# Performance work log

Hardware: AMD Instinct MI355X
Metric: run time of the kernel (lower is better)

The kernel has to match this reference:

```python
import jax, jax.numpy as jnp
import numpy as np

N_NODES = 500_000
N_EDGES = 8_000_000
NUM_GRAPHS = 512


def _glorot(key, shape):
    lim = float(np.sqrt(6.0 / (shape[0] + shape[1])))
    return jax.random.uniform(key, shape, jnp.float32, -lim, lim)


def setup_inputs() -> dict:
    key = jax.random.key(0)
    ks = jax.random.split(key, 10)
    x = jax.random.normal(ks[0], (N_NODES, 3), jnp.float32)
    edge_index = jax.random.randint(ks[1], (2, N_EDGES), 0, N_NODES, jnp.int64)
    batch = jnp.sort(jax.random.randint(ks[2], (N_NODES,), 0, NUM_GRAPHS, jnp.int64))
    return {
        "x": x,
        "edge_index": edge_index,
        "batch": batch,
        # GCNConv weights stored [in, out]; bias [out]
        "W1": _glorot(ks[3], (3, 16)),
        "b1": jnp.zeros((16,), jnp.float32),
        "W2": _glorot(ks[4], (16, 32)),
        "b2": jnp.zeros((32,), jnp.float32),
        "fW1": _glorot(ks[5], (32, 64)),
        "fb1": jnp.zeros((64,), jnp.float32),
        "fW2": _glorot(ks[6], (64, 3)),
        "fb2": jnp.zeros((3,), jnp.float32),
    }


def _gcn_conv(x, edge_index, W, b):
    n = x.shape[0]
    src, dst = edge_index[0], edge_index[1]
    h = x @ W  # [N, out]
    ones = jnp.ones((edge_index.shape[1],), h.dtype)
    deg = jax.ops.segment_sum(ones, dst, num_segments=n) + 1.0  # in-degree + self loop
    dinv = jax.lax.rsqrt(deg)
    norm = dinv[src] * dinv[dst]  # [E]
    agg = jax.ops.segment_sum(norm[:, None] * h[src], dst, num_segments=n)
    # self-loop contribution: norm_ii = dinv_i^2
    return agg + (dinv * dinv)[:, None] * h + b


def reference(x, edge_index, batch, W1, b1, W2, b2, fW1, fb1, fW2, fb2):
    h = jax.nn.relu(_gcn_conv(x, edge_index, W1, b1))
    h = jax.nn.relu(_gcn_conv(h, edge_index, W2, b2))
    # global_mean_pool over graph ids
    sums = jax.ops.segment_sum(h, batch, num_segments=NUM_GRAPHS)
    cnts = jax.ops.segment_sum(jnp.ones((h.shape[0],), h.dtype), batch, num_segments=NUM_GRAPHS)
    pooled = sums / jnp.maximum(cnts, 1.0)[:, None]  # [G, 32]
    z = jax.nn.relu(pooled @ fW1 + fb1)
    z = z @ fW2 + fb2
    return jax.nn.log_softmax(z, axis=1)
```

## Files before the change

kernel.cpp:

```cpp
#include <hip/hip_runtime.h>
#include <hip/hip_bf16.h>

constexpr int N_NODES    = 500000;
constexpr int N_EDGES    = 8000000;
constexpr int NUM_GRAPHS = 512;

constexpr int BSHIFT = 11;
constexpr int BSIZE  = 1 << BSHIFT;
constexpr int NBKT   = (N_NODES + BSIZE - 1) / BSIZE;
constexpr int EPB    = 8192;
constexpr int NBLK_A = (N_EDGES + EPB - 1) / EPB;
constexpr int NH     = NBKT * NBLK_A;
constexpr int SCAN_B = 256;
constexpr int NSB    = (NH + SCAN_B - 1) / SCAN_B;
constexpr int TSH    = 16;
constexpr int CAP    = 20480;

__device__ __forceinline__ float bf_lo(unsigned u) { return __uint_as_float(u << 16); }
__device__ __forceinline__ float bf_hi(unsigned u) { return __uint_as_float(u & 0xFFFF0000u); }
__device__ __forceinline__ unsigned short f2bf(float f) {
  unsigned u = __float_as_uint(f);
  return (unsigned short)((u + 0x7FFFu + ((u >> 16) & 1u)) >> 16);
}
__device__ __forceinline__ unsigned packbf(float a, float b) {
  return (unsigned)f2bf(a) | ((unsigned)f2bf(b) << 16);
}

__device__ __forceinline__ unsigned f2e4m3(float x) {
  x = fminf(x, 448.0f);
  unsigned xb = __float_as_uint(x);
  int e = (int)(xb >> 23) - 127;
  if (e < -6) {
    int m = (int)rintf(x * 512.0f);
    return (m <= 7) ? (unsigned)m : 0x08u;
  }
  unsigned lsb = (xb >> 20) & 1;
  unsigned r = xb + 0x7FFFFu + lsb;
  int e2 = (int)(r >> 23) - 127;
  unsigned m3 = (r >> 20) & 7;
  return (unsigned)(((e2 + 7) << 3) | m3);
}
__device__ __forceinline__ float e4m3f(unsigned b) {
  unsigned e = (b >> 3) & 0xF, m = b & 7;
  float norm = __uint_as_float(((e + 120u) << 23) | (m << 20));
  float den = (float)m * 0.001953125f;
  return e ? norm : den;
}

__global__ void k_hist(const int* __restrict__ dst, int* __restrict__ H) {
  __shared__ int h[NBKT];
  for (int i = threadIdx.x; i < NBKT; i += blockDim.x) h[i] = 0;
  __syncthreads();
  int e0 = blockIdx.x * EPB;
  int e1 = min(e0 + EPB, N_EDGES);
  for (int e = e0 + threadIdx.x; e < e1; e += blockDim.x)
    atomicAdd(&h[dst[e] >> BSHIFT], 1);
  __syncthreads();
  for (int i = threadIdx.x; i < NBKT; i += blockDim.x)
    H[i * NBLK_A + blockIdx.x] = h[i];
}

__global__ void k_scan1(const int* __restrict__ in, int* __restrict__ out,
                        int* __restrict__ bsum, int n) {
  __shared__ int tmp[SCAN_B];
  int t = threadIdx.x;
  int i = blockIdx.x * SCAN_B + t;
  int v = (i < n) ? in[i] : 0;
  tmp[t] = v;
  __syncthreads();
  for (int off = 1; off < SCAN_B; off <<= 1) {
    int a = (t >= off) ? tmp[t - off] : 0;
    __syncthreads();
    tmp[t] += a;
    __syncthreads();
  }
  if (i < n) out[i] = tmp[t] - v;
  if (t == SCAN_B - 1) bsum[blockIdx.x] = tmp[t];
}

__global__ void k_scan2(int* __restrict__ bsum, int nb) {
  __shared__ int tmp[SCAN_B];
  int t = threadIdx.x;
  int carry = 0;
  for (int base = 0; base < nb; base += SCAN_B) {
    int i = base + t;
    int v = (i < nb) ? bsum[i] : 0;
    tmp[t] = v;
    __syncthreads();
    for (int off = 1; off < SCAN_B; off <<= 1) {
      int a = (t >= off) ? tmp[t - off] : 0;
      __syncthreads();
      tmp[t] += a;
      __syncthreads();
    }
    if (i < nb) bsum[i] = carry + tmp[t] - v;
    carry += tmp[SCAN_B - 1];
    __syncthreads();
  }
}

__device__ __forceinline__ int s_at(const int* Sarr, const int* bsum, int idx) {
  return Sarr[idx] + bsum[idx >> 8];
}

__global__ void k_scatter_bkt(const int* __restrict__ src, const int* __restrict__ dst,
                              const int* __restrict__ Sarr, const int* __restrict__ bsum,
                              int* __restrict__ pairs) {
  __shared__ int lcnt[256];
  __shared__ int lofs[256];
  __shared__ int base[256];
  __shared__ int pout[EPB];
  __shared__ unsigned char bout[EPB];
  int t = threadIdx.x;
  int blk = blockIdx.x;
  int e0 = blk * EPB;
  int e1 = min(e0 + EPB, N_EDGES);
  int ne = e1 - e0;
  lcnt[t] = 0;
  __syncthreads();
  for (int e = e0 + t; e < e1; e += 256)
    atomicAdd(&lcnt[dst[e] >> BSHIFT], 1);
  __syncthreads();
  lofs[t] = lcnt[t];
  __syncthreads();
  for (int off = 1; off < 256; off <<= 1) {
    int v = (t >= off) ? lofs[t - off] : 0;
    __syncthreads();
    lofs[t] += v;
    __syncthreads();
  }
  lofs[t] -= lcnt[t];
  base[t] = (t < NBKT) ? s_at(Sarr, bsum, t * NBLK_A + blk) : 0;
  lcnt[t] = 0;
  __syncthreads();
  for (int e = e0 + t; e < e1; e += 256) {
    int d = dst[e], s = src[e];
    int b = d >> BSHIFT;
    int r = atomicAdd(&lcnt[b], 1);
    int q = lofs[b] + r;
    pout[q] = ((d & (BSIZE - 1)) << 19) | s;
    bout[q] = (unsigned char)b;
  }
  __syncthreads();
  for (int li = t; li < ne; li += 256) {
    int b = bout[li];
    pairs[base[b] + (li - lofs[b])] = pout[li];
  }
}

__global__ void __launch_bounds__(1024)
k_csr(const int* __restrict__ pairs, const int* __restrict__ Sarr,
      const int* __restrict__ bsum, const float* __restrict__ x,
      int* __restrict__ ssrc, int* __restrict__ offs,
      float* __restrict__ dinv, unsigned* __restrict__ xsb) {
  __shared__ int hist[8192];
  __shared__ int sout[CAP];
  __shared__ int tmp[1024];
  int t = threadIdx.x;
  int bkt = blockIdx.x >> 1;
  int h = blockIdx.x & 1;
  int e0 = s_at(Sarr, bsum, bkt * NBLK_A);
  int e1 = (bkt + 1 < NBKT) ? s_at(Sarr, bsum, (bkt + 1) * NBLK_A) : N_EDGES;
#pragma unroll
  for (int j = 0; j < 8; ++j) hist[t + (j << 10)] = 0;
  __syncthreads();
  int lc = 0;
  for (int e = e0 + t; e < e1; e += 1024) {
    int p = pairs[e];
    int nl = p >> 19;
    int s = p & 0x7FFFF;
    if ((nl >> 10) == h) atomicAdd(&hist[((s >> TSH) << 10) | (nl & 1023)], 1);
    else if ((nl >> 10) == 0) lc++;
  }
  tmp[t] = lc;
  __syncthreads();
  for (int off = 512; off > 0; off >>= 1) {
    if (t < off) tmp[t] += tmp[t + off];
    __syncthreads();
  }
  int halfbase = h ? tmp[0] : 0;
  __syncthreads();
  int c[8];
  int tsum = 0;
#pragma unroll
  for (int j = 0; j < 8; ++j) { c[j] = hist[(j << 10) | t]; tsum += c[j]; }
  tmp[t] = tsum;
  __syncthreads();
  for (int off = 1; off < 1024; off <<= 1) {
    int a = (t >= off) ? tmp[t - off] : 0;
    __syncthreads();
    tmp[t] += a;
    __syncthreads();
  }
  int run = tmp[t] - tsum;
  int total = tmp[1023];
  {
    int b = run;
#pragma unroll
    for (int j = 0; j < 8; ++j) { int cc = c[j]; hist[(j << 10) | t] = b; b += cc; }
  }
  int n = (bkt << BSHIFT) + (h << 10) + t;
  if (n < N_NODES) {
    offs[n] = e0 + halfbase + run;
    float di = rsqrtf((float)tsum + 1.0f);
    dinv[n] = di;
    const float* xs = x + (size_t)n * 3;
    uint2 v = make_uint2(packbf(di * xs[0], di * xs[1]), packbf(di * xs[2], 0.0f));
    *(uint2*)(xsb + (size_t)n * 2) = v;
  }
  __syncthreads();
  int base = e0 + halfbase;
  if (total <= CAP) {
    for (int e = e0 + t; e < e1; e += 1024) {
      int p = pairs[e];
      int nl = p >> 19;
      if ((nl >> 10) != h) continue;
      int s = p & 0x7FFFF;
      int r = atomicAdd(&hist[((s >> TSH) << 10) | (nl & 1023)], 1);
      sout[r] = s;
    }
    __syncthreads();
    for (int q = t; q < total; q += 1024)
      ssrc[base + q] = sout[q];
  } else {
    for (int e = e0 + t; e < e1; e += 1024) {
      int p = pairs[e];
      int nl = p >> 19;
      if ((nl >> 10) != h) continue;
      int s = p & 0x7FFFF;
      int r = atomicAdd(&hist[((s >> TSH) << 10) | (nl & 1023)], 1);
      ssrc[base + r] = s;
    }
  }
  if (bkt == 0 && h == 0 && t == 0) offs[N_NODES] = N_EDGES;
}

__global__ void k_g1f1(const int* __restrict__ ssrc, const int* __restrict__ offs,
                       const unsigned* __restrict__ xsb, const float* __restrict__ dinv,
                       const float* __restrict__ W1, const float* __restrict__ b1,
                       unsigned* __restrict__ ub) {
  unsigned t = blockIdx.x * blockDim.x + threadIdx.x;
  unsigned n = t >> 1;
  int j = t & 1;
  if (n >= (unsigned)N_NODES) return;
  int o0 = offs[n], o1 = offs[n + 1];
  float a0 = 0.0f, a1 = 0.0f;
  int i = o0;
  for (; i + 3 < o1; i += 4) {
    int s0 = ssrc[i], s1 = ssrc[i + 1], s2 = ssrc[i + 2], s3 = ssrc[i + 3];
    unsigned q0 = xsb[(size_t)s0 * 2 + j];
    unsigned q1 = xsb[(size_t)s1 * 2 + j];
    unsigned q2 = xsb[(size_t)s2 * 2 + j];
    unsigned q3 = xsb[(size_t)s3 * 2 + j];
    a0 += bf_lo(q0) + bf_lo(q1) + bf_lo(q2) + bf_lo(q3);
    a1 += bf_hi(q0) + bf_hi(q1) + bf_hi(q2) + bf_hi(q3);
  }
  for (; i < o1; ++i) {
    unsigned q = xsb[(size_t)ssrc[i] * 2 + j];
    a0 += bf_lo(q); a1 += bf_hi(q);
  }
  float oth0 = __shfl_xor(a0, 1);
  float oth1 = __shfl_xor(a1, 1);
  float A0 = j ? oth0 : a0;
  float A1v = j ? oth1 : a1;
  float A2v = j ? a0 : oth0;
  float di = dinv[n];
  uint2 xq = *(const uint2*)&xsb[(size_t)n * 2];
  float t0 = di * (A0 + bf_lo(xq.x));
  float t1 = di * (A1v + bf_hi(xq.x));
  float t2 = di * (A2v + bf_lo(xq.y));
  unsigned w0 = 0, w1 = 0;
#pragma unroll
  for (int q8 = 0; q8 < 4; ++q8) {
    int f = 8 * j + 2 * q8;
    float v0 = t0 * W1[f]     + t1 * W1[16 + f]     + t2 * W1[32 + f]     + b1[f];
    float v1 = t0 * W1[f + 1] + t1 * W1[16 + f + 1] + t2 * W1[32 + f + 1] + b1[f + 1];
    unsigned pb = f2e4m3(di * fmaxf(v0, 0.0f)) | (f2e4m3(di * fmaxf(v1, 0.0f)) << 8);
    if (q8 < 2) w0 |= pb << (16 * q8); else w1 |= pb << (16 * (q8 - 2));
  }
  *(uint2*)&ub[(size_t)n * 4 + j * 2] = make_uint2(w0, w1);
}

__global__ void k_gather2(const int* __restrict__ ssrc, const int* __restrict__ offs,
                          const unsigned* __restrict__ ub, float* __restrict__ A2) {
  __shared__ float lut[128];
  if (threadIdx.x < 128) lut[threadIdx.x] = e4m3f(threadIdx.x);
  __syncthreads();
  unsigned t = blockIdx.x * blockDim.x + threadIdx.x;
  unsigned n = t >> 2;
  int j = t & 3;
  if (n >= (unsigned)N_NODES) return;
  int o0 = offs[n], o1 = offs[n + 1];
  unsigned qs = ub[(size_t)n * 4 + j];
  float a0 = lut[qs & 0x7F];
  float a1 = lut[(qs >> 8) & 0x7F];
  float a2 = lut[(qs >> 16) & 0x7F];
  float a3 = lut[(qs >> 24) & 0x7F];
  int i = o0;
  for (; i + 1 < o1; i += 2) {
    int s0 = ssrc[i], s1 = ssrc[i + 1];
    unsigned q0 = ub[(size_t)s0 * 4 + j];
    unsigned q1 = ub[(size_t)s1 * 4 + j];
    a0 += lut[q0 & 0x7F]         + lut[q1 & 0x7F];
    a1 += lut[(q0 >> 8) & 0x7F]  + lut[(q1 >> 8) & 0x7F];
    a2 += lut[(q0 >> 16) & 0x7F] + lut[(q1 >> 16) & 0x7F];
    a3 += lut[(q0 >> 24) & 0x7F] + lut[(q1 >> 24) & 0x7F];
  }
  if (i < o1) {
    unsigned q = ub[(size_t)ssrc[i] * 4 + j];
    a0 += lut[q & 0x7F];
    a1 += lut[(q >> 8) & 0x7F];
    a2 += lut[(q >> 16) & 0x7F];
    a3 += lut[(q >> 24) & 0x7F];
  }
  *(float4*)&A2[(size_t)n * 16 + j * 4] = make_float4(a0, a1, a2, a3);
}

__global__ void k_pool2(const float* __restrict__ A2,
                        const float* __restrict__ W2, const float* __restrict__ b2,
                        const float* __restrict__ dinv, const int* __restrict__ batch,
                        float* __restrict__ sums) {
  int f = threadIdx.x & 31, sub = threadIdx.x >> 5;
  int n0 = blockIdx.x * 128 + sub * 16;
  int n1 = min(n0 + 16, N_NODES);
  if (n0 >= n1) return;
  float w2col[16];
#pragma unroll
  for (int k = 0; k < 16; ++k) w2col[k] = W2[k * 32 + f];
  float bf = b2[f];
  int cur = batch[n0];
  float acc = 0.0f;
  for (int n = n0; n < n1; ++n) {
    int g = batch[n];
    if (g != cur) { atomicAdd(&sums[(size_t)cur * 32 + f], acc); acc = 0.0f; cur = g; }
    const float4* a2p = (const float4*)(A2 + (size_t)n * 16);
    float4 aa0 = a2p[0], aa1 = a2p[1], aa2 = a2p[2], aa3 = a2p[3];
    float v = aa0.x * w2col[0]  + aa0.y * w2col[1]  + aa0.z * w2col[2]  + aa0.w * w2col[3]
            + aa1.x * w2col[4]  + aa1.y * w2col[5]  + aa1.z * w2col[6]  + aa1.w * w2col[7]
            + aa2.x * w2col[8]  + aa2.y * w2col[9]  + aa2.z * w2col[10] + aa2.w * w2col[11]
            + aa3.x * w2col[12] + aa3.y * w2col[13] + aa3.z * w2col[14] + aa3.w * w2col[15];
    v = dinv[n] * v + bf;
    acc += fmaxf(v, 0.0f);
  }
  atomicAdd(&sums[(size_t)cur * 32 + f], acc);
}

__global__ void k_mlp(const float* __restrict__ sums, const int* __restrict__ batch,
                      const float* __restrict__ fW1, const float* __restrict__ fb1,
                      const float* __restrict__ fW2, const float* __restrict__ fb2,
                      float* __restrict__ out) {
  __shared__ float w1s[32 * 64];
  __shared__ float w2s[64 * 3];
  __shared__ float b1s[64];
  __shared__ float b2s[3];
  for (int i = threadIdx.x; i < 32 * 64; i += blockDim.x) w1s[i] = fW1[i];
  for (int i = threadIdx.x; i < 64 * 3; i += blockDim.x) w2s[i] = fW2[i];
  for (int i = threadIdx.x; i < 64; i += blockDim.x) b1s[i] = fb1[i];
  for (int i = threadIdx.x; i < 3; i += blockDim.x) b2s[i] = fb2[i];
  __syncthreads();
  int g = blockIdx.x * blockDim.x + threadIdx.x;
  if (g >= NUM_GRAPHS) return;
  int lo = 0, hi = N_NODES;
  while (lo < hi) { int mid = (lo + hi) >> 1; if (batch[mid] < g) lo = mid + 1; else hi = mid; }
  int s0 = lo;
  int lo2 = s0, hi2 = N_NODES;
  while (lo2 < hi2) { int mid = (lo2 + hi2) >> 1; if (batch[mid] < g + 1) lo2 = mid + 1; else hi2 = mid; }
  float c = fmaxf((float)(lo2 - s0), 1.0f);
  float p[32];
#pragma unroll
  for (int i = 0; i < 32; ++i) p[i] = sums[(size_t)g * 32 + i] / c;
  float z2[3] = {b2s[0], b2s[1], b2s[2]};
  for (int j = 0; j < 64; ++j) {
    float a = b1s[j];
#pragma unroll
    for (int i = 0; i < 32; ++i) a += p[i] * w1s[i * 64 + j];
    a = fmaxf(a, 0.0f);
#pragma unroll
    for (int k = 0; k < 3; ++k) z2[k] += a * w2s[j * 3 + k];
  }
  float m = fmaxf(fmaxf(z2[0], z2[1]), z2[2]);
  float l = logf(expf(z2[0] - m) + expf(z2[1] - m) + expf(z2[2] - m));
#pragma unroll
  for (int k = 0; k < 3; ++k) out[(size_t)g * 3 + k] = z2[k] - m - l;
}

extern "C" void kernel_launch(void* const* d_in, const int* in_sizes, int n_in,
                              void* d_out, int out_size, void* d_ws, size_t ws_size,
                              hipStream_t stream) {
  const float* x     = (const float*)d_in[0];
  const int*   ei    = (const int*)d_in[1];
  const int*   batch = (const int*)d_in[2];
  const float* W1    = (const float*)d_in[3];
  const float* b1    = (const float*)d_in[4];
  const float* W2    = (const float*)d_in[5];
  const float* b2    = (const float*)d_in[6];
  const float* fW1   = (const float*)d_in[7];
  const float* fb1   = (const float*)d_in[8];
  const float* fW2   = (const float*)d_in[9];
  const float* fb2   = (const float*)d_in[10];
  const int* src = ei;
  const int* dst = ei + N_EDGES;

  float* ws       = (float*)d_ws;
  float* dinv     = ws;
  unsigned* xsb   = (unsigned*)(dinv + 524288);
  unsigned* ub    = xsb + 1048576;
  float* scratch  = (float*)(ub + 4194304);
  float* sums     = scratch + 2000000;
  int* offs       = (int*)(sums + 16384);
  int* ssrc       = offs + 524288;
  int* pairs      = ssrc + 8000000;
  int* H    = (int*)scratch;
  int* Sarr = H + NH;
  int* bsum = Sarr + NH;
  float* A2 = (float*)pairs;

  hipMemsetAsync(sums, 0, (size_t)NUM_GRAPHS * 32 * 4, stream);

  const int B = 256;
  k_hist<<<NBLK_A, B, 0, stream>>>(dst, H);
  k_scan1<<<NSB, SCAN_B, 0, stream>>>(H, Sarr, bsum, NH);
  k_scan2<<<1, SCAN_B, 0, stream>>>(bsum, NSB);
  k_scatter_bkt<<<NBLK_A, B, 0, stream>>>(src, dst, Sarr, bsum, pairs);
  k_csr<<<NBKT * 2, 1024, 0, stream>>>(pairs, Sarr, bsum, x, ssrc, offs, dinv, xsb);
  k_g1f1<<<((size_t)N_NODES * 2 + B - 1) / B, B, 0, stream>>>(ssrc, offs, xsb, dinv, W1, b1, ub);
  k_gather2<<<((size_t)N_NODES * 4 + B - 1) / B, B, 0, stream>>>(ssrc, offs, ub, A2);
  k_pool2<<<(N_NODES + 127) / 128, B, 0, stream>>>(A2, W2, b2, dinv, batch, sums);
  k_mlp<<<(NUM_GRAPHS + B - 1) / B, B, 0, stream>>>(sums, batch, fW1, fb1, fW2, fb2, (float*)d_out);
}
```

Before: 366.1 us.

## Use 1024-node buckets and reuse global histogram in bucket scatter

```diff
diff --git a/kernel.cpp b/kernel.cpp
--- a/kernel.cpp
+++ b/kernel.cpp
@@ -5,7 +5,7 @@
 constexpr int N_EDGES    = 8000000;
 constexpr int NUM_GRAPHS = 512;
 
-constexpr int BSHIFT = 11;
+constexpr int BSHIFT = 10;
 constexpr int BSIZE  = 1 << BSHIFT;
 constexpr int NBKT   = (N_NODES + BSIZE - 1) / BSIZE;
 constexpr int EPB    = 8192;
@@ -103,46 +103,44 @@
   return Sarr[idx] + bsum[idx >> 8];
 }
 
-__global__ void k_scatter_bkt(const int* __restrict__ src, const int* __restrict__ dst,
-                              const int* __restrict__ Sarr, const int* __restrict__ bsum,
-                              int* __restrict__ pairs) {
-  __shared__ int lcnt[256];
-  __shared__ int lofs[256];
-  __shared__ int base[256];
+__global__ void __launch_bounds__(512)
+k_scatter_bkt(const int* __restrict__ src, const int* __restrict__ dst,
+              const int* __restrict__ H, const int* __restrict__ Sarr,
+              const int* __restrict__ bsum, int* __restrict__ pairs) {
+  __shared__ int lcnt[512];
+  __shared__ int lofs[512];
+  __shared__ int base[512];
   __shared__ int pout[EPB];
-  __shared__ unsigned char bout[EPB];
+  __shared__ unsigned short bout[EPB];
   int t = threadIdx.x;
   int blk = blockIdx.x;
   int e0 = blk * EPB;
   int e1 = min(e0 + EPB, N_EDGES);
   int ne = e1 - e0;
+  int cnt = (t < NBKT) ? H[t * NBLK_A + blk] : 0;
+  lcnt[t] = cnt;
+  lofs[t] = cnt;
+  base[t] = (t < NBKT) ? s_at(Sarr, bsum, t * NBLK_A + blk) : 0;
+  __syncthreads();
+  for (int off = 1; off < 512; off <<= 1) {
+    int v = (t >= off) ? lofs[t - off] : 0;
+    __syncthreads();
+    lofs[t] += v;
+    __syncthreads();
+  }
+  lofs[t] -= lcnt[t];
   lcnt[t] = 0;
   __syncthreads();
-  for (int e = e0 + t; e < e1; e += 256)
-    atomicAdd(&lcnt[dst[e] >> BSHIFT], 1);
-  __syncthreads();
-  lofs[t] = lcnt[t];
-  __syncthreads();
-  for (int off = 1; off < 256; off <<= 1) {
-    int v = (t >= off) ? lofs[t - off] : 0;
-    __syncthreads();
-    lofs[t] += v;
-    __syncthreads();
-  }
-  lofs[t] -= lcnt[t];
-  base[t] = (t < NBKT) ? s_at(Sarr, bsum, t * NBLK_A + blk) : 0;
-  lcnt[t] = 0;
-  __syncthreads();
-  for (int e = e0 + t; e < e1; e += 256) {
+  for (int e = e0 + t; e < e1; e += 512) {
     int d = dst[e], s = src[e];
     int b = d >> BSHIFT;
     int r = atomicAdd(&lcnt[b], 1);
     int q = lofs[b] + r;
     pout[q] = ((d & (BSIZE - 1)) << 19) | s;
-    bout[q] = (unsigned char)b;
-  }
-  __syncthreads();
-  for (int li = t; li < ne; li += 256) {
+    bout[q] = (unsigned short)b;
+  }
+  __syncthreads();
+  for (int li = t; li < ne; li += 512) {
     int b = bout[li];
     pairs[base[b] + (li - lofs[b])] = pout[li];
   }
@@ -157,28 +155,18 @@
   __shared__ int sout[CAP];
   __shared__ int tmp[1024];
   int t = threadIdx.x;
-  int bkt = blockIdx.x >> 1;
-  int h = blockIdx.x & 1;
+  int bkt = blockIdx.x;
+  int n0 = bkt << BSHIFT;
   int e0 = s_at(Sarr, bsum, bkt * NBLK_A);
   int e1 = (bkt + 1 < NBKT) ? s_at(Sarr, bsum, (bkt + 1) * NBLK_A) : N_EDGES;
+  int total = e1 - e0;
 #pragma unroll
   for (int j = 0; j < 8; ++j) hist[t + (j << 10)] = 0;
   __syncthreads();
-  int lc = 0;
   for (int e = e0 + t; e < e1; e += 1024) {
     int p = pairs[e];
-    int nl = p >> 19;
-    int s = p & 0x7FFFF;
-    if ((nl >> 10) == h) atomicAdd(&hist[((s >> TSH) << 10) | (nl & 1023)], 1);
-    else if ((nl >> 10) == 0) lc++;
-  }
-  tmp[t] = lc;
-  __syncthreads();
-  for (int off = 512; off > 0; off >>= 1) {
-    if (t < off) tmp[t] += tmp[t + off];
-    __syncthreads();
-  }
-  int halfbase = h ? tmp[0] : 0;
+    atomicAdd(&hist[(((p & 0x7FFFF) >> TSH) << 10) | (p >> 19)], 1);
+  }
   __syncthreads();
   int c[8];
   int tsum = 0;
@@ -193,15 +181,14 @@
     __syncthreads();
   }
   int run = tmp[t] - tsum;
-  int total = tmp[1023];
   {
     int b = run;
 #pragma unroll
     for (int j = 0; j < 8; ++j) { int cc = c[j]; hist[(j << 10) | t] = b; b += cc; }
   }
-  int n = (bkt << BSHIFT) + (h << 10) + t;
+  int n = n0 + t;
   if (n < N_NODES) {
-    offs[n] = e0 + halfbase + run;
+    offs[n] = e0 + run;
     float di = rsqrtf((float)tsum + 1.0f);
     dinv[n] = di;
     const float* xs = x + (size_t)n * 3;
@@ -209,30 +196,25 @@
     *(uint2*)(xsb + (size_t)n * 2) = v;
   }
   __syncthreads();
-  int base = e0 + halfbase;
   if (total <= CAP) {
     for (int e = e0 + t; e < e1; e += 1024) {
       int p = pairs[e];
-      int nl = p >> 19;
-      if ((nl >> 10) != h) continue;
       int s = p & 0x7FFFF;
-      int r = atomicAdd(&hist[((s >> TSH) << 10) | (nl & 1023)], 1);
+      int r = atomicAdd(&hist[((s >> TSH) << 10) | (p >> 19)], 1);
       sout[r] = s;
     }
     __syncthreads();
     for (int q = t; q < total; q += 1024)
-      ssrc[base + q] = sout[q];
+      ssrc[e0 + q] = sout[q];
   } else {
     for (int e = e0 + t; e < e1; e += 1024) {
       int p = pairs[e];
-      int nl = p >> 19;
-      if ((nl >> 10) != h) continue;
       int s = p & 0x7FFFF;
-      int r = atomicAdd(&hist[((s >> TSH) << 10) | (nl & 1023)], 1);
-      ssrc[base + r] = s;
+      int r = atomicAdd(&hist[((s >> TSH) << 10) | (p >> 19)], 1);
+      ssrc[e0 + r] = s;
     }
   }
-  if (bkt == 0 && h == 0 && t == 0) offs[N_NODES] = N_EDGES;
+  if (bkt == 0 && t == 0) offs[N_NODES] = N_EDGES;
 }
 
 __global__ void k_g1f1(const int* __restrict__ ssrc, const int* __restrict__ offs,
@@ -421,8 +403,8 @@
   k_hist<<<NBLK_A, B, 0, stream>>>(dst, H);
   k_scan1<<<NSB, SCAN_B, 0, stream>>>(H, Sarr, bsum, NH);
   k_scan2<<<1, SCAN_B, 0, stream>>>(bsum, NSB);
-  k_scatter_bkt<<<NBLK_A, B, 0, stream>>>(src, dst, Sarr, bsum, pairs);
-  k_csr<<<NBKT * 2, 1024, 0, stream>>>(pairs, Sarr, bsum, x, ssrc, offs, dinv, xsb);
+  k_scatter_bkt<<<NBLK_A, 512, 0, stream>>>(src, dst, H, Sarr, bsum, pairs);
+  k_csr<<<NBKT, 1024, 0, stream>>>(pairs, Sarr, bsum, x, ssrc, offs, dinv, xsb);
   k_g1f1<<<((size_t)N_NODES * 2 + B - 1) / B, B, 0, stream>>>(ssrc, offs, xsb, dinv, W1, b1, ub);
   k_gather2<<<((size_t)N_NODES * 4 + B - 1) / B, B, 0, stream>>>(ssrc, offs, ub, A2);
   k_pool2<<<(N_NODES + 127) / 128, B, 0, stream>>>(A2, W2, b2, dinv, batch, sums);
```

New measurement: 329.6 us. 1.11x faster.
